# Kernel optimization log

Hardware: AMD Instinct MI355X
Metric: run time of the kernel (lower is better)

The kernel has to match this reference:

```python
import jax, jax.numpy as jnp
import numpy as np

EMBED_DIM = 1024
NUM_HEADS = 16
HEAD_DIM = EMBED_DIM // NUM_HEADS
NUM_LANDMARKS = 64
REG = 1e-6
BATCH = 2
SEQ = 8192


def setup_inputs() -> dict:
    key = jax.random.key(0)
    ks = jax.random.split(key, 10)
    s = 0.02
    inp = {
        "query": jax.random.normal(ks[0], (BATCH, SEQ, EMBED_DIM), dtype=jnp.float32),
        "Wq": jax.random.normal(ks[1], (EMBED_DIM, EMBED_DIM), dtype=jnp.float32) * s,
        "bq": jnp.zeros((EMBED_DIM,), jnp.float32),
        "Wk": jax.random.normal(ks[2], (EMBED_DIM, EMBED_DIM), dtype=jnp.float32) * s,
        "bk": jnp.zeros((EMBED_DIM,), jnp.float32),
        "Wv": jax.random.normal(ks[3], (EMBED_DIM, EMBED_DIM), dtype=jnp.float32) * s,
        "bv": jnp.zeros((EMBED_DIM,), jnp.float32),
        "Wo": jax.random.normal(ks[4], (EMBED_DIM, EMBED_DIM), dtype=jnp.float32) * s,
        "bo": jnp.zeros((EMBED_DIM,), jnp.float32),
        "temperature": jnp.asarray(float(HEAD_DIM), jnp.float32),
        # deterministic uniform landmark selection (strided, distinct indices)
        "landmark_idx": jnp.arange(NUM_LANDMARKS, dtype=jnp.int32) * (SEQ // NUM_LANDMARKS),
    }
    return inp


def _sq_dists(X, L):
    # X: (b,h,n,d), L: (b,h,k,d) -> (b,h,n,k) squared euclidean distances
    Xn = jnp.sum(X * X, axis=-1, keepdims=True)            # (b,h,n,1)
    Ln = jnp.sum(L * L, axis=-1, keepdims=True)            # (b,h,k,1)
    XL = jnp.einsum("bhnd,bhkd->bhnk", X, L)
    return jnp.maximum(Xn + jnp.swapaxes(Ln, -2, -1) - 2.0 * XL, 0.0)


def reference(query, Wq, bq, Wk, bk, Wv, bv, Wo, bo, temperature, landmark_idx):
    b, n, _ = query.shape
    # torch Linear: x @ W.T + b
    Q = (query @ Wq.T + bq).reshape(b, n, NUM_HEADS, HEAD_DIM).transpose(0, 2, 1, 3)
    K = (query @ Wk.T + bk).reshape(b, n, NUM_HEADS, HEAD_DIM).transpose(0, 2, 1, 3)
    V = (query @ Wv.T + bv).reshape(b, n, NUM_HEADS, HEAD_DIM).transpose(0, 2, 1, 3)

    landmarks = K[:, :, landmark_idx, :]                   # (b,h,k,d)
    C_Q = _sq_dists(Q, landmarks)                          # (b,h,n,k)
    C_K = _sq_dists(K, landmarks)                          # (b,h,n,k)
    W_sq = C_K[:, :, landmark_idx, :]                      # (b,h,k,k)

    Phi_Q = jnp.exp(-C_Q / temperature)
    Phi_K = jnp.exp(-C_K / temperature)
    W_kernel = jnp.exp(-W_sq / temperature) + REG * jnp.eye(NUM_LANDMARKS, dtype=query.dtype)

    # cholesky_inverse(W) @ X == solve(W, X) for SPD W
    Z = jnp.einsum("bhnk,bhnd->bhkd", Phi_K, V)            # (b,h,k,d)
    Y = jnp.linalg.solve(W_kernel, Z)                      # (b,h,k,d)
    out_unnorm = jnp.einsum("bhnk,bhkd->bhnd", Phi_Q, Y)   # (b,h,n,d)

    Phi_K_sum = jnp.sum(Phi_K, axis=-2)[..., None]         # (b,h,k,1)
    norm = jnp.einsum("bhnk,bhko->bhno", Phi_Q, jnp.linalg.solve(W_kernel, Phi_K_sum))
    norm = jnp.maximum(norm, 1e-10)

    out = out_unnorm / norm                                # (b,h,n,d)
    out = out.transpose(0, 2, 1, 3).reshape(b, n, EMBED_DIM)
    return out @ Wo.T + bo
```

## Files before the change

### kernel.cpp

```cpp
#include <hip/hip_runtime.h>
#include <stdint.h>

typedef unsigned short u16;
typedef unsigned int u32;
typedef __attribute__((ext_vector_type(8))) __bf16 bf16x8;
typedef __attribute__((ext_vector_type(8))) u16 u16x8;
typedef __attribute__((ext_vector_type(4))) float f32x4;
typedef __attribute__((ext_vector_type(4))) u32 u32x4;

#define DEV static __device__ __forceinline__

namespace {

constexpr int NB2  = 2;
constexpr int SEQL = 8192;
constexpr int EMB  = 1024;
constexpr int HD   = 64;
constexpr int NLM  = 64;
constexpr int NTOK = NB2 * SEQL;

constexpr size_t OFF_QBF  = 0;
constexpr size_t OFF_WBF  = OFF_QBF  + 33554432;
constexpr size_t OFF_QKV  = OFF_WBF  + 8388608;
constexpr size_t OFF_ATT  = OFF_QKV  + 100663296;
constexpr size_t OFF_LAND = OFF_ATT  + 33554432;
constexpr size_t OFF_LN   = OFF_LAND + 262144;
constexpr size_t OFF_WK   = OFF_LN   + 8192;
constexpr size_t OFF_ZP   = OFF_WK   + 524288;
constexpr size_t OFF_SP   = OFF_ZP   + 4194304;
constexpr size_t OFF_YT   = OFF_SP   + 65536;

DEV u16 f2bf(float f){
  u32 u = __builtin_bit_cast(u32, f);
  u32 r = (u + 0x7FFFu + ((u >> 16) & 1u)) >> 16;
  return (u16)r;
}
DEV float bf2f(u16 h){ u32 u = ((u32)h) << 16; return __builtin_bit_cast(float, u); }
DEV u16x8 ld8(const u16* p){ return *(const u16x8*)p; }
DEV f32x4 mfma16(u16x8 a, u16x8 b, f32x4 c){
  return __builtin_amdgcn_mfma_f32_16x16x32_bf16(
      __builtin_bit_cast(bf16x8, a), __builtin_bit_cast(bf16x8, b), c, 0, 0, 0);
}
DEV void gld_lds16(void* lds, const void* g){
  __builtin_amdgcn_global_load_lds(
      (__attribute__((address_space(1))) void*)(uintptr_t)g,
      (__attribute__((address_space(3))) void*)(u32)(uintptr_t)lds,
      16, 0, 0);
}
DEV void vmwait4(){ asm volatile("s_waitcnt vmcnt(4)" ::: "memory"); }
DEV void vmwait0(){ asm volatile("s_waitcnt vmcnt(0)" ::: "memory"); }
DEV void barrier_pin(){
  __builtin_amdgcn_s_barrier();
  __builtin_amdgcn_sched_barrier(0);
}
DEV u32 swz(u32 a){ return a ^ (((a >> 7) & 7u) << 4); }
DEV float rdlane(float v, int l){
  return __builtin_bit_cast(float, __builtin_amdgcn_readlane(__builtin_bit_cast(int, v), l));
}

__global__ __launch_bounds__(256) void k_cvt(const float* __restrict__ src,
                                             u16* __restrict__ dst, int n8){
  int i = blockIdx.x * blockDim.x + threadIdx.x;
  if (i >= n8) return;
  float t[8];
  *(float4*)&t[0] = ((const float4*)src)[2*i];
  *(float4*)&t[4] = ((const float4*)src)[2*i + 1];
  u16x8 o;
  #pragma unroll
  for (int j = 0; j < 8; ++j) o[j] = f2bf(t[j]);
  *(u16x8*)&dst[(size_t)i * 8] = o;
}

template <int MODE>
__global__ __launch_bounds__(512, 2) void k_gemm256(
    const u16* __restrict__ A, const u16* __restrict__ Wb,
    const float* __restrict__ b0, const float* __restrict__ b1,
    const float* __restrict__ b2, u16* __restrict__ OutB, float* __restrict__ OutF)
{
  constexpr int NI = 8;
  __shared__ __align__(16) u16 lds[2][2][2][128*64];
  const int tid = threadIdx.x, lane = tid & 63, wv = tid >> 6;
  const int wr = wv >> 2, wc = wv & 3;
  const int fr = lane & 15, fk = (lane >> 4) * 8;

  constexpr int NBX = (MODE == 0) ? 12 : 4;
  constexpr int CPX = NBX * 64 / 8;
  const int lin = blockIdx.x + NBX * blockIdx.y;
  const int w = (lin & 7) * CPX + (lin >> 3);
  const int bxw = w % NBX, byw = w / NBX;
  const int wsel = (MODE == 0) ? (bxw >> 2) : 0;
  const int col0 = (MODE == 0) ? ((bxw & 3) * 256) : (bxw * 256);
  const int row0 = byw * 256;
  const u16* Bm = Wb + (size_t)wsel * EMB * EMB;

  int voff[2]; u32 lo_[2];
  #pragma unroll
  for (int j = 0; j < 2; ++j) {
    u32 P  = (u32)((j*8 + wv) * 1024);
    u32 Pl = P + (u32)lane * 16;
    u32 L  = swz(Pl);
    voff[j] = (int)((L >> 7) * EMB + ((L >> 1) & 63));
    lo_[j]  = P;
  }
  u32 qsw[2];
  #pragma unroll
  for (int ks = 0; ks < 2; ++ks)
    qsw[ks] = swz((u32)(fr*128 + ks*64 + fk*2));

  f32x4 acc[8][4] = {};
  u16x8 af[2][8], bfr[2][4];

  auto STAGE = [&](int buf, int mat, int half, int kt) {
    const u16* gb = (mat == 0)
      ? (A  + (size_t)(row0 + half*128) * EMB + kt*64)
      : (Bm + (size_t)(col0 + half*128) * EMB + kt*64);
    char* lb = (char*)&lds[buf][mat][half][0];
    #pragma unroll
    for (int j = 0; j < 2; ++j)
      gld_lds16(lb + lo_[j], gb + voff[j]);
  };
  auto LDA = [&](int buf, int m, int ks) -> u16x8 {
    return ld8((const u16*)((const char*)&lds[buf][0][wr][0] + m*2048 + qsw[ks]));
  };
  auto LDB = [&](int buf, int n, int ks) -> u16x8 {
    return ld8((const u16*)((const char*)&lds[buf][1][wc>>1][0]
                            + (wc&1)*8192 + n*2048 + qsw[ks]));
  };
  auto READ_LO = [&](int buf) {
    #pragma unroll
    for (int ks = 0; ks < 2; ++ks) {
      #pragma unroll
      for (int m = 0; m < 4; ++m) af[ks][m] = LDA(buf, m, ks);
      #pragma unroll
      for (int n = 0; n < 2; ++n) bfr[ks][n] = LDB(buf, n, ks);
    }
  };
  auto READ_HI = [&](int buf) {
    #pragma unroll
    for (int ks = 0; ks < 2; ++ks) {
      #pragma unroll
      for (int m = 0; m < 4; ++m) af[ks][4+m] = LDA(buf, 4+m, ks);
      #pragma unroll
      for (int n = 0; n < 2; ++n) bfr[ks][2+n] = LDB(buf, 2+n, ks);
    }
  };
  auto MFMAQ = [&](int mh, int nh) {
    __builtin_amdgcn_s_setprio(1);
    #pragma unroll
    for (int ks = 0; ks < 2; ++ks)
      #pragma unroll
      for (int m = 0; m < 4; ++m)
        #pragma unroll
        for (int n = 0; n < 2; ++n) {
          const int mi = mh*4 + m, ni = nh*2 + n;
          acc[mi][ni] = mfma16(af[ks][mi], bfr[ks][ni], acc[mi][ni]);
        }
    __builtin_amdgcn_s_setprio(0);
  };

  STAGE(0,0,0,0); STAGE(0,0,1,0); STAGE(0,1,0,0); STAGE(0,1,1,0);
  STAGE(1,0,0,1); STAGE(1,0,1,1);
  vmwait4();
  barrier_pin();

  #pragma unroll 1
  for (int it = 0; it < NI; ++it) {
    const int kt0 = 2*it;
    const bool last = (it == NI-1);
    READ_LO(0); STAGE(1,1,0,kt0+1);
    barrier_pin(); MFMAQ(0,0); barrier_pin();
    READ_HI(0); STAGE(1,1,1,kt0+1);
    barrier_pin(); MFMAQ(0,1); barrier_pin();
    if (!last) STAGE(0,0,0,kt0+2);
    barrier_pin(); MFMAQ(1,1); barrier_pin();
    if (!last) { STAGE(0,0,1,kt0+2); vmwait4(); } else { vmwait0(); }
    barrier_pin(); MFMAQ(1,0); barrier_pin();
    READ_LO(1); if (!last) STAGE(0,1,0,kt0+2);
    barrier_pin(); MFMAQ(0,0); barrier_pin();
    READ_HI(1); if (!last) STAGE(0,1,1,kt0+2);
    barrier_pin(); MFMAQ(0,1); barrier_pin();
    if (!last) STAGE(1,0,0,kt0+3);
    barrier_pin(); MFMAQ(1,1); barrier_pin();
    if (!last) { STAGE(1,0,1,kt0+3); vmwait4(); }
    barrier_pin(); MFMAQ(1,0); barrier_pin();
  }

  const int rgrp = (lane >> 4) * 4;
  if (MODE == 0) {
    const float* bias = (wsel == 0) ? b0 : ((wsel == 1) ? b1 : b2);
    u16* Out = OutB + (size_t)wsel * NTOK * EMB;
    #pragma unroll
    for (int m = 0; m < 8; ++m) {
      const int r0 = row0 + wr*128 + m*16 + rgrp;
      #pragma unroll
      for (int n = 0; n < 4; ++n) {
        const int c = col0 + wc*64 + n*16 + fr;
        const float bb = bias[c];
        #pragma unroll
        for (int j = 0; j < 4; ++j)
          Out[(size_t)(r0 + j)*EMB + c] = f2bf(acc[m][n][j] + bb);
      }
    }
  } else {
    #pragma unroll
    for (int m = 0; m < 8; ++m) {
      const int r0 = row0 + wr*128 + m*16 + rgrp;
      #pragma unroll
      for (int n = 0; n < 4; ++n) {
        const int c = col0 + wc*64 + n*16 + fr;
        const float bb = b0[c];
        #pragma unroll
        for (int j = 0; j < 4; ++j)
          OutF[(size_t)(r0 + j)*EMB + c] = acc[m][n][j] + bb;
      }
    }
  }
}

__global__ __launch_bounds__(256) void k_land(
    const u16* __restrict__ QKV, const int* __restrict__ lidx,
    const float* __restrict__ tempp,
    u16* __restrict__ land, float* __restrict__ lnorm, float* __restrict__ wker)
{
  const int bh = blockIdx.x;
  const int b = bh >> 4, h = bh & 15;
  const int tid = threadIdx.x;
  __shared__ __align__(16) u16 Ls[NLM*HD];
  __shared__ float Lns[NLM];
  const u16* Kp = QKV + (size_t)NTOK*EMB + (size_t)b*SEQL*EMB + h*HD;
  {
    const int l = tid >> 2, p = tid & 3;
    const int row = lidx[l];
    const u16* src = Kp + (size_t)row*EMB + p*16;
    *(u32x4*)&Ls[l*64 + p*16]     = *(const u32x4*)src;
    *(u32x4*)&Ls[l*64 + p*16 + 8] = *(const u32x4*)(src + 8);
  }
  __syncthreads();
  if (tid < 64) {
    float s = 0;
    for (int d = 0; d < 64; ++d) { float v = bf2f(Ls[tid*64 + d]); s += v*v; }
    Lns[tid] = s;
  }
  __syncthreads();
  const float invt = 1.0f / tempp[0];
  for (int e = tid; e < 4096; e += 256) {
    const int i = e >> 6, j = e & 63;
    float dot = 0;
    for (int d = 0; d < 64; ++d) dot += bf2f(Ls[i*64 + d]) * bf2f(Ls[j*64 + d]);
    const float c = fmaxf(Lns[i] + Lns[j] - 2.0f*dot, 0.0f);
    wker[(size_t)bh*4096 + e] = __expf(-c * invt) + (i == j ? 1e-6f : 0.0f);
  }
  for (int e = tid; e < 4096; e += 256) land[(size_t)bh*4096 + e] = Ls[e];
  if (tid < 64) lnorm[bh*64 + tid] = Lns[tid];
}

__global__ __launch_bounds__(64) void k_inv(float* __restrict__ wker)
{
  const int bh = blockIdx.x;
  const int lane = threadIdx.x;
  float* wp = wker + (size_t)bh * 4096;
  float w[64];
  #pragma unroll
  for (int r = 0; r < 64; ++r) w[r] = wp[r*64 + lane];
  #pragma unroll 1
  for (int cp = 0; cp < 64; ++cp) {
    const float diag = rdlane(w[0], cp);
    const float inv  = 1.0f / diag;
    const float oneh = (lane == cp) ? 1.0f : 0.0f;
    const float pj = w[0] * inv + oneh * inv;
    const float newpiv = pj - oneh;
    #pragma unroll
    for (int r = 1; r < 64; ++r) {
      const float f = rdlane(w[r], cp);
      w[r-1] = w[r] - f * pj;
    }
    w[63] = newpiv;
  }
  #pragma unroll
  for (int r = 0; r < 64; ++r) wp[r*64 + lane] = w[r];
}

__global__ __launch_bounds__(256) void k_apply(
    const float* __restrict__ winv, const float* __restrict__ ZP,
    const float* __restrict__ SP, u16* __restrict__ YT)
{
  const int bh = blockIdx.x;
  const int tid = threadIdx.x;
  __shared__ float Wi[64][65];
  __shared__ float Rh[64][66];
  for (int e = tid; e < 4096; e += 256) Wi[e >> 6][e & 63] = winv[(size_t)bh*4096 + e];
  for (int e = tid; e < 4096; e += 256) {
    float s = 0;
    #pragma unroll
    for (int c = 0; c < 8; ++c) s += ZP[((size_t)bh*8 + c)*4096 + e];
    Rh[e >> 6][e & 63] = s;
  }
  if (tid < 64) {
    float s = 0;
    #pragma unroll
    for (int c = 0; c < 8; ++c) s += SP[(bh*8 + c)*64 + tid];
    Rh[tid][64] = s;
  }
  __syncthreads();
  u16* yt = YT + (size_t)bh * 80 * 64;
  const int l = tid & 63, de0 = tid >> 6;
  for (int de = de0; de < 65; de += 4) {
    float s = 0;
    #pragma unroll
    for (int k = 0; k < 64; ++k) s += Wi[l][k] * Rh[k][de];
    yt[de*64 + l] = f2bf(s);
  }
  for (int e = tid; e < 15*64; e += 256) yt[65*64 + e] = 0;
}

__global__ __launch_bounds__(256) void k_phik(
    const u16* __restrict__ QKV, const u16* __restrict__ land,
    const float* __restrict__ lnorm, const float* __restrict__ tempp,
    float* __restrict__ ZP, float* __restrict__ SP)
{
  const int chunk = blockIdx.x;
  const int bh = blockIdx.y;
  const int b = bh >> 4, h = bh & 15;
  const int tid = threadIdx.x, lane = tid & 63, wv = tid >> 6;
  const int fr = lane & 15, fk = (lane >> 4) * 8, rgrp = (lane >> 4) * 4;
  __shared__ __align__(16) u16 Ls[NLM*HD];
  __shared__ float Lns[NLM];
  __shared__ __align__(16) u16 phiT[4][NLM*32];
  __shared__ float zbuf[NLM*HD];
  __shared__ float wsum[4][NLM];

  for (int i = tid; i < 512; i += 256)
    *(u32x4*)&Ls[i*8] = *(const u32x4*)&land[(size_t)bh*4096 + (size_t)i*8];
  if (tid < 64) Lns[tid] = lnorm[bh*64 + tid];
  __syncthreads();

  const float invt = 1.0f / tempp[0];
  const u16* Kp = QKV + (size_t)NTOK*EMB   + (size_t)b*SEQL*EMB + h*HD;
  const u16* Vp = QKV + (size_t)2*NTOK*EMB + (size_t)b*SEQL*EMB + h*HD;

  u16x8 bl[2][4];
  #pragma unroll
  for (int ks = 0; ks < 2; ++ks)
    #pragma unroll
    for (int lt = 0; lt < 4; ++lt)
      bl[ks][lt] = ld8(&Ls[(lt*16 + fr)*64 + ks*32 + fk]);

  f32x4 zacc[4][4] = {};
  float pacc[4] = {0.f, 0.f, 0.f, 0.f};
  const int n0 = chunk*1024 + wv*256;

  for (int g = 0; g < 8; ++g) {
    const int ng = n0 + g*32;
    u16x8 ak[2][2];
    #pragma unroll
    for (int rt = 0; rt < 2; ++rt)
      #pragma unroll
      for (int ks = 0; ks < 2; ++ks)
        ak[rt][ks] = ld8(Kp + (size_t)(ng + rt*16 + fr)*EMB + ks*32 + fk);
    float kn[2];
    #pragma unroll
    for (int rt = 0; rt < 2; ++rt) {
      float s = 0;
      #pragma unroll
      for (int ks = 0; ks < 2; ++ks)
        #pragma unroll
        for (int jj = 0; jj < 8; ++jj) { float v = bf2f(ak[rt][ks][jj]); s += v*v; }
      s += __shfl_xor(s, 16); s += __shfl_xor(s, 32);
      kn[rt] = s;
    }
    f32x4 ckl[2][4] = {};
    #pragma unroll
    for (int ks = 0; ks < 2; ++ks)
      #pragma unroll
      for (int rt = 0; rt < 2; ++rt)
        #pragma unroll
        for (int lt = 0; lt < 4; ++lt)
          ckl[rt][lt] = mfma16(ak[rt][ks], bl[ks][lt], ckl[rt][lt]);
    #pragma unroll
    for (int rt = 0; rt < 2; ++rt)
      #pragma unroll
      for (int lt = 0; lt < 4; ++lt)
        #pragma unroll
        for (int j = 0; j < 4; ++j) {
          const float knr = __shfl(kn[rt], rgrp + j);
          const float c = fmaxf(knr + Lns[lt*16 + fr] - 2.0f*ckl[rt][lt][j], 0.0f);
          const float ph = __expf(-c * invt);
          pacc[lt] += ph;
          phiT[wv][(lt*16 + fr)*32 + rt*16 + rgrp + j] = f2bf(ph);
        }
    u16x8 ap[4];
    #pragma unroll
    for (int lt = 0; lt < 4; ++lt) ap[lt] = ld8(&phiT[wv][(lt*16 + fr)*32 + fk]);
    #pragma unroll
    for (int dt = 0; dt < 4; ++dt) {
      u16x8 bvu;
      #pragma unroll
      for (int jj = 0; jj < 8; ++jj)
        bvu[jj] = Vp[(size_t)(ng + fk + jj)*EMB + dt*16 + fr];
      #pragma unroll
      for (int lt = 0; lt < 4; ++lt)
        zacc[lt][dt] = mfma16(ap[lt], bvu, zacc[lt][dt]);
    }
  }
  #pragma unroll
  for (int lt = 0; lt < 4; ++lt) {
    float s = pacc[lt];
    s += __shfl_xor(s, 16); s += __shfl_xor(s, 32);
    if (lane < 16) wsum[wv][lt*16 + lane] = s;
  }
  for (int w = 0; w < 4; ++w) {
    __syncthreads();
    if (wv == w) {
      #pragma unroll
      for (int lt = 0; lt < 4; ++lt)
        #pragma unroll
        for (int dt = 0; dt < 4; ++dt)
          #pragma unroll
          for (int j = 0; j < 4; ++j) {
            const int l = lt*16 + rgrp + j, d = dt*16 + fr;
            if (w == 0) zbuf[l*64 + d]  = zacc[lt][dt][j];
            else        zbuf[l*64 + d] += zacc[lt][dt][j];
          }
    }
  }
  __syncthreads();
  float* zp = ZP + ((size_t)bh*8 + chunk)*4096;
  for (int e = tid; e < 4096; e += 256) zp[e] = zbuf[e];
  if (tid < 64)
    SP[(bh*8 + chunk)*64 + tid] = wsum[0][tid] + wsum[1][tid] + wsum[2][tid] + wsum[3][tid];
}

__global__ __launch_bounds__(256) void k_out_attn(
    const u16* __restrict__ QKV, const u16* __restrict__ land,
    const float* __restrict__ lnorm, const float* __restrict__ tempp,
    const u16* __restrict__ YT, u16* __restrict__ attn)
{
  const int chunk = blockIdx.x;
  const int bh = blockIdx.y;
  const int b = bh >> 4, h = bh & 15;
  const int tid = threadIdx.x, lane = tid & 63, wv = tid >> 6;
  const int fr = lane & 15, fk = (lane >> 4) * 8, rgrp = (lane >> 4) * 4;
  __shared__ __align__(16) u16 Ls[NLM*HD];
  __shared__ float Lns[NLM];
  __shared__ __align__(16) u16 YTs[80*64];
  __shared__ __align__(16) u16 phin[4][32*64];

  for (int i = tid; i < 512; i += 256)
    *(u32x4*)&Ls[i*8] = *(const u32x4*)&land[(size_t)bh*4096 + (size_t)i*8];
  for (int i = tid; i < 640; i += 256)
    *(u32x4*)&YTs[i*8] = *(const u32x4*)&YT[(size_t)bh*5120 + (size_t)i*8];
  if (tid < 64) Lns[tid] = lnorm[bh*64 + tid];
  __syncthreads();

  const float invt = 1.0f / tempp[0];
  u16x8 bl[2][4], byf[2][5];
  #pragma unroll
  for (int ks = 0; ks < 2; ++ks) {
    #pragma unroll
    for (int lt = 0; lt < 4; ++lt) bl[ks][lt] = ld8(&Ls[(lt*16 + fr)*64 + ks*32 + fk]);
    #pragma unroll
    for (int dt = 0; dt < 5; ++dt) byf[ks][dt] = ld8(&YTs[(dt*16 + fr)*64 + ks*32 + fk]);
  }
  const u16* Qp = QKV + (size_t)b*SEQL*EMB + h*HD;
  const int n0 = chunk*128 + wv*32;
  u16x8 aq[2][2];
  #pragma unroll
  for (int rt = 0; rt < 2; ++rt)
    #pragma unroll
    for (int ks = 0; ks < 2; ++ks)
      aq[rt][ks] = ld8(Qp + (size_t)(n0 + rt*16 + fr)*EMB + ks*32 + fk);
  float qn[2];
  #pragma unroll
  for (int rt = 0; rt < 2; ++rt) {
    float s = 0;
    #pragma unroll
    for (int ks = 0; ks < 2; ++ks)
      #pragma unroll
      for (int jj = 0; jj < 8; ++jj) { float v = bf2f(aq[rt][ks][jj]); s += v*v; }
    s += __shfl_xor(s, 16); s += __shfl_xor(s, 32);
    qn[rt] = s;
  }
  f32x4 cql[2][4] = {};
  #pragma unroll
  for (int ks = 0; ks < 2; ++ks)
    #pragma unroll
    for (int rt = 0; rt < 2; ++rt)
      #pragma unroll
      for (int lt = 0; lt < 4; ++lt)
        cql[rt][lt] = mfma16(aq[rt][ks], bl[ks][lt], cql[rt][lt]);
  #pragma unroll
  for (int rt = 0; rt < 2; ++rt)
    #pragma unroll
    for (int lt = 0; lt < 4; ++lt)
      #pragma unroll
      for (int j = 0; j < 4; ++j) {
        const float knr = __shfl(qn[rt], rgrp + j);
        const float c = fmaxf(knr + Lns[lt*16 + fr] - 2.0f*cql[rt][lt][j], 0.0f);
        phin[wv][(rt*16 + rgrp + j)*64 + lt*16 + fr] = f2bf(__expf(-c * invt));
      }
  u16x8 ap[2][2];
  #pragma unroll
  for (int rt = 0; rt < 2; ++rt)
    #pragma unroll
    for (int ks = 0; ks < 2; ++ks)
      ap[rt][ks] = ld8(&phin[wv][(rt*16 + fr)*64 + ks*32 + fk]);
  f32x4 o[2][5] = {};
  #pragma unroll
  for (int ks = 0; ks < 2; ++ks)
    #pragma unroll
    for (int rt = 0; rt < 2; ++rt)
      #pragma unroll
      for (int dt = 0; dt < 5; ++dt)
        o[rt][dt] = mfma16(ap[rt][ks], byf[ks][dt], o[rt][dt]);
  u16* Apt = attn + (size_t)b*SEQL*EMB + h*HD;
  #pragma unroll
  for (int rt = 0; rt < 2; ++rt)
    #pragma unroll
    for (int j = 0; j < 4; ++j) {
      const float nv = fmaxf(__shfl(o[rt][4][j], lane & 48), 1e-10f);
      const float rn = 1.0f / nv;
      const int row = n0 + rt*16 + rgrp + j;
      #pragma unroll
      for (int dt = 0; dt < 4; ++dt)
        Apt[(size_t)row*EMB + dt*16 + fr] = f2bf(o[rt][dt][j] * rn);
    }
}

}

extern "C" void kernel_launch(void* const* d_in, const int* in_sizes, int n_in,
                              void* d_out, int out_size, void* d_ws, size_t ws_size,
                              hipStream_t stream) {
  (void)in_sizes; (void)n_in; (void)out_size; (void)ws_size;
  const float* query = (const float*)d_in[0];
  const float* Wq = (const float*)d_in[1];
  const float* bq = (const float*)d_in[2];
  const float* Wk = (const float*)d_in[3];
  const float* bk = (const float*)d_in[4];
  const float* Wv = (const float*)d_in[5];
  const float* bv = (const float*)d_in[6];
  const float* Wo = (const float*)d_in[7];
  const float* bo = (const float*)d_in[8];
  const float* temp = (const float*)d_in[9];
  const int*   lidx = (const int*)d_in[10];
  float* out = (float*)d_out;
  char* ws = (char*)d_ws;

  u16* qbf   = (u16*)(ws + OFF_QBF);
  u16* wbf   = (u16*)(ws + OFF_WBF);
  u16* qkv   = (u16*)(ws + OFF_QKV);
  u16* attn  = (u16*)(ws + OFF_ATT);
  u16* land  = (u16*)(ws + OFF_LAND);
  float* lnorm = (float*)(ws + OFF_LN);
  float* wker  = (float*)(ws + OFF_WK);
  float* ZP  = (float*)(ws + OFF_ZP);
  float* SP  = (float*)(ws + OFF_SP);
  u16* YT    = (u16*)(ws + OFF_YT);

  k_cvt<<<NTOK*EMB/8/256, 256, 0, stream>>>(query, qbf, NTOK*EMB/8);
  k_cvt<<<EMB*EMB/8/256, 256, 0, stream>>>(Wq, wbf + 0*EMB*EMB, EMB*EMB/8);
  k_cvt<<<EMB*EMB/8/256, 256, 0, stream>>>(Wk, wbf + 1*EMB*EMB, EMB*EMB/8);
  k_cvt<<<EMB*EMB/8/256, 256, 0, stream>>>(Wv, wbf + 2*EMB*EMB, EMB*EMB/8);
  k_cvt<<<EMB*EMB/8/256, 256, 0, stream>>>(Wo, wbf + 3*EMB*EMB, EMB*EMB/8);

  k_gemm256<0><<<dim3(12, 64), 512, 0, stream>>>(qbf, wbf, bq, bk, bv, qkv, nullptr);
  k_land<<<32, 256, 0, stream>>>(qkv, lidx, temp, land, lnorm, wker);
  k_inv<<<32, 64, 0, stream>>>(wker);
  k_phik<<<dim3(8, 32), 256, 0, stream>>>(qkv, land, lnorm, temp, ZP, SP);
  k_apply<<<32, 256, 0, stream>>>(wker, ZP, SP, YT);
  k_out_attn<<<dim3(64, 32), 256, 0, stream>>>(qkv, land, lnorm, temp, YT, attn);
  k_gemm256<1><<<dim3(4, 64), 512, 0, stream>>>(attn, wbf + 3*EMB*EMB, bo, nullptr,
                                                nullptr, nullptr, out);
}
```

Before: 283.3 us.

## Merge conversion launches, fuse inversion into landmark kernel, coarsen GEMM pipeline stages

```diff
diff --git a/kernel.cpp b/kernel.cpp
--- a/kernel.cpp
+++ b/kernel.cpp
@@ -58,17 +58,28 @@
   return __builtin_bit_cast(float, __builtin_amdgcn_readlane(__builtin_bit_cast(int, v), l));
 }
 
-__global__ __launch_bounds__(256) void k_cvt(const float* __restrict__ src,
-                                             u16* __restrict__ dst, int n8){
-  int i = blockIdx.x * blockDim.x + threadIdx.x;
-  if (i >= n8) return;
+__global__ __launch_bounds__(256) void k_cvt_all(
+    const float* __restrict__ q,  const float* __restrict__ wq,
+    const float* __restrict__ wk, const float* __restrict__ wv,
+    const float* __restrict__ wo, u16* __restrict__ qbf, u16* __restrict__ wbf)
+{
+  const int b = blockIdx.x;
+  const float* src; u16* dst; int g;
+  if (b < 8192) {
+    src = q; dst = qbf; g = b*256 + threadIdx.x;
+  } else {
+    const int w = (b - 8192) >> 9;
+    src = (w == 0) ? wq : (w == 1) ? wk : (w == 2) ? wv : wo;
+    dst = wbf + (size_t)w * EMB * EMB;
+    g = ((b - 8192) & 511)*256 + threadIdx.x;
+  }
   float t[8];
-  *(float4*)&t[0] = ((const float4*)src)[2*i];
-  *(float4*)&t[4] = ((const float4*)src)[2*i + 1];
+  *(float4*)&t[0] = ((const float4*)src)[2*g];
+  *(float4*)&t[4] = ((const float4*)src)[2*g + 1];
   u16x8 o;
   #pragma unroll
   for (int j = 0; j < 8; ++j) o[j] = f2bf(t[j]);
-  *(u16x8*)&dst[(size_t)i * 8] = o;
+  *(u16x8*)&dst[(size_t)g * 8] = o;
 }
 
 template <int MODE>
@@ -171,18 +182,15 @@
     barrier_pin(); MFMAQ(0,0); barrier_pin();
     READ_HI(0); STAGE(1,1,1,kt0+1);
     barrier_pin(); MFMAQ(0,1); barrier_pin();
-    if (!last) STAGE(0,0,0,kt0+2);
-    barrier_pin(); MFMAQ(1,1); barrier_pin();
-    if (!last) { STAGE(0,0,1,kt0+2); vmwait4(); } else { vmwait0(); }
-    barrier_pin(); MFMAQ(1,0); barrier_pin();
+    if (!last) { STAGE(0,0,0,kt0+2); STAGE(0,0,1,kt0+2); vmwait4(); }
+    else       { vmwait0(); }
+    barrier_pin(); MFMAQ(1,1); MFMAQ(1,0); barrier_pin();
     READ_LO(1); if (!last) STAGE(0,1,0,kt0+2);
     barrier_pin(); MFMAQ(0,0); barrier_pin();
     READ_HI(1); if (!last) STAGE(0,1,1,kt0+2);
     barrier_pin(); MFMAQ(0,1); barrier_pin();
-    if (!last) STAGE(1,0,0,kt0+3);
-    barrier_pin(); MFMAQ(1,1); barrier_pin();
-    if (!last) { STAGE(1,0,1,kt0+3); vmwait4(); }
-    barrier_pin(); MFMAQ(1,0); barrier_pin();
+    if (!last) { STAGE(1,0,0,kt0+3); STAGE(1,0,1,kt0+3); vmwait4(); }
+    barrier_pin(); MFMAQ(1,1); MFMAQ(1,0); barrier_pin();
   }
 
   const int rgrp = (lane >> 4) * 4;
@@ -220,13 +228,14 @@
 __global__ __launch_bounds__(256) void k_land(
     const u16* __restrict__ QKV, const int* __restrict__ lidx,
     const float* __restrict__ tempp,
-    u16* __restrict__ land, float* __restrict__ lnorm, float* __restrict__ wker)
+    u16* __restrict__ land, float* __restrict__ lnorm, float* __restrict__ winv)
 {
   const int bh = blockIdx.x;
   const int b = bh >> 4, h = bh & 15;
   const int tid = threadIdx.x;
   __shared__ __align__(16) u16 Ls[NLM*HD];
   __shared__ float Lns[NLM];
+  __shared__ float Wm[64][65];
   const u16* Kp = QKV + (size_t)NTOK*EMB + (size_t)b*SEQL*EMB + h*HD;
   {
     const int l = tid >> 2, p = tid & 3;
@@ -248,36 +257,34 @@
     float dot = 0;
     for (int d = 0; d < 64; ++d) dot += bf2f(Ls[i*64 + d]) * bf2f(Ls[j*64 + d]);
     const float c = fmaxf(Lns[i] + Lns[j] - 2.0f*dot, 0.0f);
-    wker[(size_t)bh*4096 + e] = __expf(-c * invt) + (i == j ? 1e-6f : 0.0f);
+    Wm[i][j] = __expf(-c * invt) + (i == j ? 1e-6f : 0.0f);
   }
   for (int e = tid; e < 4096; e += 256) land[(size_t)bh*4096 + e] = Ls[e];
   if (tid < 64) lnorm[bh*64 + tid] = Lns[tid];
-}
-
-__global__ __launch_bounds__(64) void k_inv(float* __restrict__ wker)
-{
-  const int bh = blockIdx.x;
-  const int lane = threadIdx.x;
-  float* wp = wker + (size_t)bh * 4096;
-  float w[64];
-  #pragma unroll
-  for (int r = 0; r < 64; ++r) w[r] = wp[r*64 + lane];
-  #pragma unroll 1
-  for (int cp = 0; cp < 64; ++cp) {
-    const float diag = rdlane(w[0], cp);
-    const float inv  = 1.0f / diag;
-    const float oneh = (lane == cp) ? 1.0f : 0.0f;
-    const float pj = w[0] * inv + oneh * inv;
-    const float newpiv = pj - oneh;
-    #pragma unroll
-    for (int r = 1; r < 64; ++r) {
-      const float f = rdlane(w[r], cp);
-      w[r-1] = w[r] - f * pj;
-    }
-    w[63] = newpiv;
-  }
-  #pragma unroll
-  for (int r = 0; r < 64; ++r) wp[r*64 + lane] = w[r];
+  __syncthreads();
+  if (tid < 64) {
+    const int lane = tid;
+    float w[64];
+    #pragma unroll
+    for (int r = 0; r < 64; ++r) w[r] = Wm[r][lane];
+    #pragma unroll 1
+    for (int cp = 0; cp < 64; ++cp) {
+      const float diag = rdlane(w[0], cp);
+      const float inv  = 1.0f / diag;
+      const float oneh = (lane == cp) ? 1.0f : 0.0f;
+      const float pj = w[0] * inv + oneh * inv;
+      const float newpiv = pj - oneh;
+      #pragma unroll
+      for (int r = 1; r < 64; ++r) {
+        const float f = rdlane(w[r], cp);
+        w[r-1] = w[r] - f * pj;
+      }
+      w[63] = newpiv;
+    }
+    float* wp = winv + (size_t)bh * 4096;
+    #pragma unroll
+    for (int r = 0; r < 64; ++r) wp[r*64 + lane] = w[r];
+  }
 }
 
 __global__ __launch_bounds__(256) void k_apply(
@@ -552,22 +559,17 @@
   u16* attn  = (u16*)(ws + OFF_ATT);
   u16* land  = (u16*)(ws + OFF_LAND);
   float* lnorm = (float*)(ws + OFF_LN);
-  float* wker  = (float*)(ws + OFF_WK);
+  float* winv  = (float*)(ws + OFF_WK);
   float* ZP  = (float*)(ws + OFF_ZP);
   float* SP  = (float*)(ws + OFF_SP);
   u16* YT    = (u16*)(ws + OFF_YT);
 
-  k_cvt<<<NTOK*EMB/8/256, 256, 0, stream>>>(query, qbf, NTOK*EMB/8);
-  k_cvt<<<EMB*EMB/8/256, 256, 0, stream>>>(Wq, wbf + 0*EMB*EMB, EMB*EMB/8);
-  k_cvt<<<EMB*EMB/8/256, 256, 0, stream>>>(Wk, wbf + 1*EMB*EMB, EMB*EMB/8);
-  k_cvt<<<EMB*EMB/8/256, 256, 0, stream>>>(Wv, wbf + 2*EMB*EMB, EMB*EMB/8);
-  k_cvt<<<EMB*EMB/8/256, 256, 0, stream>>>(Wo, wbf + 3*EMB*EMB, EMB*EMB/8);
+  k_cvt_all<<<8192 + 4*512, 256, 0, stream>>>(query, Wq, Wk, Wv, Wo, qbf, wbf);
 
   k_gemm256<0><<<dim3(12, 64), 512, 0, stream>>>(qbf, wbf, bq, bk, bv, qkv, nullptr);
-  k_land<<<32, 256, 0, stream>>>(qkv, lidx, temp, land, lnorm, wker);
-  k_inv<<<32, 64, 0, stream>>>(wker);
+  k_land<<<32, 256, 0, stream>>>(qkv, lidx, temp, land, lnorm, winv);
   k_phik<<<dim3(8, 32), 256, 0, stream>>>(qkv, land, lnorm, temp, ZP, SP);
-  k_apply<<<32, 256, 0, stream>>>(wker, ZP, SP, YT);
+  k_apply<<<32, 256, 0, stream>>>(winv, ZP, SP, YT);
   k_out_attn<<<dim3(64, 32), 256, 0, stream>>>(qkv, land, lnorm, temp, YT, attn);
   k_gemm256<1><<<dim3(4, 64), 512, 0, stream>>>(attn, wbf + 3*EMB*EMB, bo, nullptr,
                                                 nullptr, nullptr, out);
```

Measured after the change: 267.9 us. -5.4%, faster.
